# Kernel tuning notes

Hardware: AMD Instinct MI355X
Metric: run time of the kernel (lower is better)

The kernel has to match this reference:

```python
import jax, jax.numpy as jnp
import numpy as np

B, IN, H, L = 128, 256, 1024, 256
nA, nB = H // 2, (H - 1) // 2        # pairs per A-layer / B-layer
LB = L // 2
LA = L - LB                           # A layers come first when L is odd
PI = float(np.pi)


def setup_inputs() -> dict:
    key = jax.random.key(0)
    ks = jax.random.split(key, 14)
    u = lambda k, shp: jax.random.uniform(k, shp, minval=-PI, maxval=PI)
    return {
        "inputsR": jax.random.normal(ks[0], (B, IN), dtype=jnp.float32),
        "inputsI": jax.random.normal(ks[1], (B, IN), dtype=jnp.float32),
        "stateR": jax.random.normal(ks[2], (B, H), dtype=jnp.float32),
        "stateI": jax.random.normal(ks[3], (B, H), dtype=jnp.float32),
        # CLinear params (init_scale=0.01 inside RNNCellCmplx)
        "weightR": 0.01 * jax.random.normal(ks[4], (H, IN), dtype=jnp.float32),
        "weightI": 0.01 * jax.random.normal(ks[5], (H, IN), dtype=jnp.float32),
        "biasR": 0.01 * jax.random.normal(ks[6], (H,), dtype=jnp.float32),
        "biasI": 0.01 * jax.random.normal(ks[7], (H,), dtype=jnp.float32),
        # Clements mesh angles, uniform(-pi, pi)
        "angleA0": u(ks[8], (LA, nA)),
        "angleA1": u(ks[9], (LA, nA)),
        "angleB0": u(ks[10], (LB, nB)),
        "angleB1": u(ks[11], (LB, nB)),
        # diagonal phase + modReLU bias (both init to zero)
        "omega": jnp.zeros((H,), dtype=jnp.float32),
        "mod_bias": jnp.zeros((H,), dtype=jnp.float32),
    }


def _mzi(ar, ai, br, bi, th0, th1):
    """PSDC MZI on channel pairs: phase shifter e^{i*th0} on arm a, then a
    directional coupler with coupling angle th1 (unitary 2x2)."""
    c0, s0 = jnp.cos(th0), jnp.sin(th0)
    pr = c0 * ar - s0 * ai          # p = e^{i th0} * a
    pi_ = s0 * ar + c0 * ai
    c, s = jnp.cos(th1), jnp.sin(th1)
    oar = c * pr - s * bi           # a' = cos*p + i sin*b
    oai = c * pi_ + s * br
    obr = c * br - s * pi_          # b' = i sin*p + cos*b
    obi = c * bi + s * pr
    return oar, oai, obr, obi


def _layerA(xr, xi, t0, t1):
    Bs, N = xr.shape
    oar, oai, obr, obi = _mzi(xr[:, 0::2], xi[:, 0::2], xr[:, 1::2], xi[:, 1::2], t0, t1)
    xr = jnp.stack([oar, obr], axis=-1).reshape(Bs, N)
    xi = jnp.stack([oai, obi], axis=-1).reshape(Bs, N)
    return xr, xi


def _layerB(xr, xi, t0, t1):
    Bs, N = xr.shape  # pairs (1,2),(3,4),... ; channels 0 and N-1 pass through
    oar, oai, obr, obi = _mzi(xr[:, 1:-1:2], xi[:, 1:-1:2], xr[:, 2::2], xi[:, 2::2], t0, t1)
    midr = jnp.stack([oar, obr], axis=-1).reshape(Bs, N - 2)
    midi = jnp.stack([oai, obi], axis=-1).reshape(Bs, N - 2)
    xr = jnp.concatenate([xr[:, :1], midr, xr[:, -1:]], axis=1)
    xi = jnp.concatenate([xi[:, :1], midi, xi[:, -1:]], axis=1)
    return xr, xi


def _clements(xr, xi, A0, A1, B0, B1):
    def step(carry, ang):
        cr, ci = carry
        a0, a1, b0, b1 = ang
        cr, ci = _layerA(cr, ci, a0, a1)
        cr, ci = _layerB(cr, ci, b0, b1)
        return (cr, ci), None
    (xr, xi), _ = jax.lax.scan(step, (xr, xi), (A0[:LB], A1[:LB], B0, B1))
    for k in range(LB, LA):  # trailing A layer when num_layers is odd (static)
        xr, xi = _layerA(xr, xi, A0[k], A1[k])
    return xr, xi


def _forward(inputsR, inputsI, stateR, stateI, weightR, weightI, biasR, biasI,
             angleA0, angleA1, angleB0, angleB1, omega, mod_bias):
    # CLinear: complex y = W x + b
    ihR = inputsR @ weightR.T - inputsI @ weightI.T + biasR
    ihI = inputsR @ weightI.T + inputsI @ weightR.T + biasI
    # Clements unitary mesh on hidden state
    hr, hi = _clements(stateR, stateI, angleA0, angleA1, angleB0, angleB1)
    # diagonal phase e^{i omega}
    co, so = jnp.cos(omega), jnp.sin(omega)
    hhR = co * hr - so * hi
    hhI = so * hr + co * hi
    # complex add
    zr = ihR + hhR
    zi = ihI + hhI
    # modReLU: relu(|z| + b) * z / |z|
    mag = jnp.sqrt(zr * zr + zi * zi)
    scale = jax.nn.relu(mag + mod_bias) / jnp.maximum(mag, 1e-8)
    return jnp.stack([scale * zr, scale * zi])  # (2, B, H)


def reference(inputsR, inputsI, stateR, stateI, weightR, weightI, biasR, biasI,
              angleA0, angleA1, angleB0, angleB1, omega, mod_bias):
    return _forward(inputsR, inputsI, stateR, stateI, weightR, weightI, biasR, biasI,
                    angleA0, angleA1, angleB0, angleB1, omega, mod_bias)
```

## Files before the change

### kernel.cpp

```cpp
#include <hip/hip_runtime.h>
#include <math.h>

typedef float v2 __attribute__((ext_vector_type(2)));

#define NBATCH 128
#define NIN    256
#define NH     1024
#define NSTEPS 128
#define NB     511

#define TAB_F4_PER_L 1024
#define IH_OFF (NSTEPS * TAB_F4_PER_L * 4)

#define GEMM_BLOCKS 256
#define TRIG_BLOCKS 512

static __device__ __forceinline__ v2 to2(float a, float b) { v2 r; r.x = a; r.y = b; return r; }

__global__ __launch_bounds__(256) void prep_kernel(
    const float* __restrict__ inR, const float* __restrict__ inI,
    const float* __restrict__ wR,  const float* __restrict__ wI,
    const float* __restrict__ biasR, const float* __restrict__ biasI,
    const float* __restrict__ A0, const float* __restrict__ A1,
    const float* __restrict__ B0, const float* __restrict__ B1,
    float* __restrict__ ws)
{
    __shared__ v2 xs[256][17];
    __shared__ v2 wsh[32][34];

    if (blockIdx.x >= GEMM_BLOCKS) {
        int idx = (blockIdx.x - GEMM_BLOCKS) * 256 + threadIdx.x;
        int l = idx >> 10;
        int s = idx & 1023;
        int j = s >> 6, lane = s & 63;
        float a0, a1;
        bool ident = false;
        if (j < 8) {
            int p = 8 * lane + j;
            a0 = A0[l * 512 + p]; a1 = A1[l * 512 + p];
        } else {
            int p = 8 * lane + (j - 8);
            if (p < NB) { a0 = B0[l * NB + p]; a1 = B1[l * NB + p]; }
            else ident = true;
        }
        float4 v;
        if (ident) v = make_float4(1.f, 0.f, 1.f, 0.f);
        else {
            float s0, c0, s1, c1;
            __sincosf(a0, &s0, &c0);
            __sincosf(a1, &s1, &c1);
            v = make_float4(c0, s0, c1, s1);
        }
        ((float4*)ws)[l * TAB_F4_PER_L + j * 64 + lane] = v;
        return;
    }

    const int ht = blockIdx.x >> 3, bt = blockIdx.x & 7;
    const int h0 = ht * 32, b0 = bt * 16;
    const int tid = threadIdx.x;

    {
        int b = tid >> 4, k4 = tid & 15;
#pragma unroll
        for (int p = 0; p < 4; ++p) {
            int k0 = p * 64 + k4 * 4;
            float4 vr = *(const float4*)(inR + (b0 + b) * NIN + k0);
            float4 vi = *(const float4*)(inI + (b0 + b) * NIN + k0);
            xs[k0 + 0][b] = to2(vr.x, vi.x);
            xs[k0 + 1][b] = to2(vr.y, vi.y);
            xs[k0 + 2][b] = to2(vr.z, vi.z);
            xs[k0 + 3][b] = to2(vr.w, vi.w);
        }
    }

    const int hg = tid & 15, bl = tid >> 4;
    v2 acc0 = to2(0.f, 0.f), acc1 = to2(0.f, 0.f);

    for (int c = 0; c < 8; ++c) {
        __syncthreads();
        {
            int hh = tid >> 3, k4 = tid & 7;
            float4 vr = *(const float4*)(wR + (h0 + hh) * NIN + c * 32 + k4 * 4);
            float4 vi = *(const float4*)(wI + (h0 + hh) * NIN + c * 32 + k4 * 4);
            wsh[k4 * 4 + 0][hh] = to2(vr.x, vi.x);
            wsh[k4 * 4 + 1][hh] = to2(vr.y, vi.y);
            wsh[k4 * 4 + 2][hh] = to2(vr.z, vi.z);
            wsh[k4 * 4 + 3][hh] = to2(vr.w, vi.w);
        }
        __syncthreads();
#pragma unroll
        for (int k = 0; k < 32; ++k) {
            float4 wv = *(const float4*)&wsh[k][hg * 2];
            v2 w0 = to2(wv.x, wv.y), w1 = to2(wv.z, wv.w);
            v2 xv = xs[c * 32 + k][bl];
            acc0 += to2(xv.x, xv.x) * w0 + to2(xv.y, xv.y) * to2(-w0.y, w0.x);
            acc1 += to2(xv.x, xv.x) * w1 + to2(xv.y, xv.y) * to2(-w1.y, w1.x);
        }
    }
    int h = h0 + hg * 2, b = b0 + bl;
    acc0 += to2(biasR[h], biasI[h]);
    acc1 += to2(biasR[h + 1], biasI[h + 1]);
    ((float4*)(ws + IH_OFF))[b * 512 + (h >> 1)] =
        make_float4(acc0.x, acc0.y, acc1.x, acc1.y);
}

__device__ __forceinline__ void mzi(const float4 t, v2& a, v2& b)
{
    v2 P  = to2(t.x, t.y) * to2(a.x, a.x) + to2(-t.y, t.x) * to2(a.y, a.y);
    v2 na = to2(t.z, t.z) * P + to2(-t.w, t.w) * to2(b.y, b.x);
    b     = to2(t.z, t.z) * b + to2(-t.w, t.w) * to2(P.y, P.x);
    a = na;
}

__device__ __forceinline__ void step(v2* x, const float4* T, int lane)
{
    mzi(T[0], x[0], x[1]);
    mzi(T[7], x[14], x[15]);
    float rc0r  = __shfl_down(x[0].x, 1, 64);
    float rc0i  = __shfl_down(x[0].y, 1, 64);
    float lc15r = __shfl_up(x[15].x, 1, 64);
    float lc15i = __shfl_up(x[15].y, 1, 64);
    float blx = __shfl_up(T[15].x, 1, 64);
    float bly = __shfl_up(T[15].y, 1, 64);
    float blz = __shfl_up(T[15].z, 1, 64);
    float blw = __shfl_up(T[15].w, 1, 64);
    if (lane == 0) { blx = 1.f; bly = 0.f; blz = 1.f; blw = 0.f; }
#pragma unroll
    for (int j = 1; j < 7; ++j) mzi(T[j], x[2 * j], x[2 * j + 1]);
#pragma unroll
    for (int j = 0; j < 7; ++j) mzi(T[8 + j], x[2 * j + 1], x[2 * j + 2]);
    {
        const float4 t = T[15];
        v2 P = to2(t.x, t.y) * to2(x[15].x, x[15].x) + to2(-t.y, t.x) * to2(x[15].y, x[15].y);
        x[15] = to2(t.z, t.z) * P + to2(-t.w, t.w) * to2(rc0i, rc0r);
    }
    {
        v2 P = to2(blx, bly) * to2(lc15r, lc15r) + to2(-bly, blx) * to2(lc15i, lc15i);
        x[0] = to2(blz, blz) * x[0] + to2(-blw, blw) * to2(P.y, P.x);
    }
}

#define LOADL(T, l)                                                       \
    do {                                                                  \
        const float4* _p = tab + (l) * TAB_F4_PER_L + lane;               \
        _Pragma("unroll") for (int _j = 0; _j < 16; ++_j)                 \
            T[_j] = _p[_j * 64];                                          \
    } while (0)

__global__ __launch_bounds__(64, 1) void mesh_kernel(
    const float* __restrict__ stateR, const float* __restrict__ stateI,
    const float* __restrict__ omega,  const float* __restrict__ mod_bias,
    const float* __restrict__ ws, float* __restrict__ out)
{
    const int b = blockIdx.x;
    const int lane = threadIdx.x;
    const float4* tab = (const float4*)ws;

    v2 x[16];
    {
        const float4* sr4 = (const float4*)(stateR + b * NH + lane * 16);
        const float4* si4 = (const float4*)(stateI + b * NH + lane * 16);
#pragma unroll
        for (int q = 0; q < 4; ++q) {
            float4 r = sr4[q], i = si4[q];
            x[4 * q + 0] = to2(r.x, i.x);
            x[4 * q + 1] = to2(r.y, i.y);
            x[4 * q + 2] = to2(r.z, i.z);
            x[4 * q + 3] = to2(r.w, i.w);
        }
    }

    float4 Ta[16], Tb[16];
    LOADL(Ta, 0);
    for (int l = 0; l < NSTEPS; l += 2) {
        LOADL(Tb, l + 1);
        __builtin_amdgcn_sched_barrier(0);
        step(x, Ta, lane);
        {
            int ln = (l + 2 < NSTEPS) ? l + 2 : NSTEPS - 1;
            LOADL(Ta, ln);
        }
        __builtin_amdgcn_sched_barrier(0);
        step(x, Tb, lane);
    }

    float om[16], mb[16];
#pragma unroll
    for (int q = 0; q < 4; ++q) {
        float4 o = ((const float4*)(omega + lane * 16))[q];
        float4 m = ((const float4*)(mod_bias + lane * 16))[q];
        om[4 * q] = o.x; om[4 * q + 1] = o.y; om[4 * q + 2] = o.z; om[4 * q + 3] = o.w;
        mb[4 * q] = m.x; mb[4 * q + 1] = m.y; mb[4 * q + 2] = m.z; mb[4 * q + 3] = m.w;
    }
    float o0[16], o1[16];
    const float4* ihp = (const float4*)(ws + IH_OFF + b * NH * 2) + lane * 8;
#pragma unroll
    for (int q = 0; q < 8; ++q) {
        float4 ih2 = ihp[q];
#pragma unroll
        for (int e = 0; e < 2; ++e) {
            int j = 2 * q + e;
            float ihr = (e == 0) ? ih2.x : ih2.z;
            float ihi = (e == 0) ? ih2.y : ih2.w;
            float so, co;
            __sincosf(om[j], &so, &co);
            float zr = ihr + co * x[j].x - so * x[j].y;
            float zi = ihi + so * x[j].x + co * x[j].y;
            float mag = sqrtf(zr * zr + zi * zi);
            float sc = fmaxf(mag + mb[j], 0.f) / fmaxf(mag, 1e-8f);
            o0[j] = sc * zr;
            o1[j] = sc * zi;
        }
    }
#pragma unroll
    for (int q = 0; q < 4; ++q) {
        ((float4*)(out + b * NH + lane * 16))[q] =
            make_float4(o0[4 * q], o0[4 * q + 1], o0[4 * q + 2], o0[4 * q + 3]);
        ((float4*)(out + NBATCH * NH + b * NH + lane * 16))[q] =
            make_float4(o1[4 * q], o1[4 * q + 1], o1[4 * q + 2], o1[4 * q + 3]);
    }
}

extern "C" void kernel_launch(void* const* d_in, const int* in_sizes, int n_in,
                              void* d_out, int out_size, void* d_ws, size_t ws_size,
                              hipStream_t stream)
{
    const float* inputsR = (const float*)d_in[0];
    const float* inputsI = (const float*)d_in[1];
    const float* stateR  = (const float*)d_in[2];
    const float* stateI  = (const float*)d_in[3];
    const float* weightR = (const float*)d_in[4];
    const float* weightI = (const float*)d_in[5];
    const float* biasR   = (const float*)d_in[6];
    const float* biasI   = (const float*)d_in[7];
    const float* angleA0 = (const float*)d_in[8];
    const float* angleA1 = (const float*)d_in[9];
    const float* angleB0 = (const float*)d_in[10];
    const float* angleB1 = (const float*)d_in[11];
    const float* omega   = (const float*)d_in[12];
    const float* mod_b   = (const float*)d_in[13];
    float* ws = (float*)d_ws;
    float* out = (float*)d_out;

    hipLaunchKernelGGL(prep_kernel, dim3(GEMM_BLOCKS + TRIG_BLOCKS), dim3(256),
                       0, stream, inputsR, inputsI, weightR, weightI,
                       biasR, biasI, angleA0, angleA1, angleB0, angleB1, ws);
    hipLaunchKernelGGL(mesh_kernel, dim3(NBATCH), dim3(64), 0, stream,
                       stateR, stateI, omega, mod_b, ws, out);
}
```

Measured before the change: 159.6 us.

## Stream mesh layer tables into LDS with async global_load_lds, 3-deep prefetch

Replaces the register double-buffered per-layer table loads with direct global-to-LDS async loads into a 4-slot ring, keeping three layers in flight ahead of compute with explicit vmcnt waits. The goal is to hide global memory latency of the per-step rotation tables behind the serial mesh steps and to free the 32 registers used by two table buffers. It adds an LDS read per step and relies on hand-coded vmcnt counts, with no barrier needed since each lane reads its own slot.

```diff
diff --git a/kernel.cpp b/kernel.cpp
--- a/kernel.cpp
+++ b/kernel.cpp
@@ -140,18 +140,16 @@
     }
 }
 
-#define LOADL(T, l)                                                       \
-    do {                                                                  \
-        const float4* _p = tab + (l) * TAB_F4_PER_L + lane;               \
-        _Pragma("unroll") for (int _j = 0; _j < 16; ++_j)                 \
-            T[_j] = _p[_j * 64];                                          \
-    } while (0)
+#define GLOBAL_AS const __attribute__((address_space(1))) void*
+#define LDS_AS    __attribute__((address_space(3))) void*
 
 __global__ __launch_bounds__(64, 1) void mesh_kernel(
     const float* __restrict__ stateR, const float* __restrict__ stateI,
     const float* __restrict__ omega,  const float* __restrict__ mod_bias,
     const float* __restrict__ ws, float* __restrict__ out)
 {
+    __shared__ float4 smem[4][16][64];
+
     const int b = blockIdx.x;
     const int lane = threadIdx.x;
     const float4* tab = (const float4*)ws;
@@ -170,18 +168,35 @@
         }
     }
 
-    float4 Ta[16], Tb[16];
-    LOADL(Ta, 0);
-    for (int l = 0; l < NSTEPS; l += 2) {
-        LOADL(Tb, l + 1);
-        __builtin_amdgcn_sched_barrier(0);
-        step(x, Ta, lane);
-        {
-            int ln = (l + 2 < NSTEPS) ? l + 2 : NSTEPS - 1;
-            LOADL(Ta, ln);
-        }
-        __builtin_amdgcn_sched_barrier(0);
-        step(x, Tb, lane);
+#define ISSUE_LAYER(l)                                                        \
+    do {                                                                      \
+        const float4* _src = tab + (l) * TAB_F4_PER_L + lane;                 \
+        _Pragma("unroll") for (int _j = 0; _j < 16; ++_j)                     \
+            __builtin_amdgcn_global_load_lds(                                 \
+                (GLOBAL_AS)(_src + _j * 64),                                  \
+                (LDS_AS)&smem[(l) & 3][_j][0], 16, 0, 0);                     \
+    } while (0)
+
+    ISSUE_LAYER(0);
+    ISSUE_LAYER(1);
+    ISSUE_LAYER(2);
+
+    for (int l = 0; l < NSTEPS; ++l) {
+        if (l < NSTEPS - 3) {
+            ISSUE_LAYER(l + 3);
+            asm volatile("s_waitcnt vmcnt(48)" ::: "memory");
+        } else if (l == NSTEPS - 3) {
+            asm volatile("s_waitcnt vmcnt(32)" ::: "memory");
+        } else if (l == NSTEPS - 2) {
+            asm volatile("s_waitcnt vmcnt(16)" ::: "memory");
+        } else {
+            asm volatile("s_waitcnt vmcnt(0)" ::: "memory");
+        }
+        float4 T[16];
+        const int slot = l & 3;
+#pragma unroll
+        for (int j = 0; j < 16; ++j) T[j] = smem[slot][j][lane];
+        step(x, T, lane);
     }
 
     float om[16], mb[16];
```

New measurement: 211.7 us. +32.6%, slower.
